# Performance work log

Measured on AMD Instinct MI355X. Metric: run time of the kernel, lower is better.

## Reference

```python
import jax, jax.numpy as jnp
import numpy as np

BS, L, D, ITEM_NUM = 64, 100, 64, 100000  # batch, max_seq_len, embedding_dim, item vocab
NEG_INF = -10000.0


def setup_inputs() -> dict:
    key = jax.random.key(0)
    k1, k2, k3, k4, k5 = jax.random.split(key, 5)
    N = BS * (L + 1)
    return {
        "prec_vec": jax.random.normal(k1, (BS * L, D), jnp.float32),
        "score_embs": jax.random.normal(k2, (N, D), jnp.float32),
        "pop_prob_list": jax.random.uniform(k3, (ITEM_NUM + 1,), jnp.float32, 0.01, 1.0),
        "sample_items_id": jax.random.randint(k4, (N,), 0, ITEM_NUM + 1, dtype=jnp.int32),
        "log_mask": jax.random.randint(k5, (BS, L), 0, 2, dtype=jnp.int32),
    }


def reference(prec_vec, score_embs, pop_prob_list, sample_items_id, log_mask):
    bs, L_ = log_mask.shape
    N = sample_items_id.shape[0]  # bs * (L+1)

    # debiased in-batch sampled-softmax logits: [bs*L, N]
    debias = jnp.log(pop_prob_list[sample_items_id])
    logits = jnp.matmul(prec_vec, score_embs.T) - debias[None, :]

    # column mask: padded positions (log_mask==0); last position of each seq always valid
    col_valid = jnp.concatenate(
        [log_mask, jnp.ones((bs, 1), log_mask.dtype)], axis=1
    ).reshape(-1)  # [N]
    logits = jnp.where(col_valid[None, :] == 0, NEG_INF, logits)

    # duplicate-item mask: dup[i, k] = any item in sequence i equals sample_items_id[k]
    id_list = sample_items_id.reshape(bs, L_ + 1)
    dup = (sample_items_id[None, None, :] == id_list[:, :, None]).any(axis=1)  # [bs, N]

    # targets: label for (i, j) is flat column i*(L+1) + j + 1
    tgt = jnp.arange(bs)[:, None] * (L_ + 1) + jnp.arange(L_)[None, :] + 1  # [bs, L]

    # apply dup mask per (i, j) but never mask the row's own target column
    not_target = jnp.arange(N)[None, None, :] != tgt[:, :, None]  # [bs, L, N]
    mask3 = dup[:, None, :] & not_target
    logits3 = jnp.where(mask3, NEG_INF, logits.reshape(bs, L_, N))

    # masked cross-entropy, mean over valid (log_mask != 0) rows
    logits2 = logits3.reshape(bs * L_, N)
    labels = tgt.reshape(-1)
    logp = jax.nn.log_softmax(logits2, axis=-1)
    nll = -jnp.take_along_axis(logp, labels[:, None], axis=1)[:, 0]  # [bs*L]
    w = (log_mask.reshape(-1) != 0).astype(logits2.dtype)
    return jnp.sum(nll * w) / jnp.sum(w)
```

## Files before the change

kernel.cpp:

```cpp
#include <hip/hip_runtime.h>

#define NEG_INF (-10000.0f)
#define L_SEQ   100
#define N_COLS  6464
#define D_      64
#define N_ROWS  6400
#define NS      16

#define OFF_PS  0
#define OFF_XT  409600
#define OFF_ACC 435200

typedef __attribute__((ext_vector_type(8))) short short8;
typedef __attribute__((ext_vector_type(4))) float f32x4;
union F8 { short8 v; unsigned short u[8]; unsigned w[4]; };

__device__ __forceinline__ unsigned short f2bf(float f) {
  unsigned u = __float_as_uint(f);
  return (unsigned short)((u + 0x7FFFu + ((u >> 16) & 1u)) >> 16);
}
__device__ __forceinline__ unsigned packbf(float lo, float hi) {
  return (__float_as_uint(hi) & 0xFFFF0000u) | (__float_as_uint(lo) >> 16);
}

__global__ __launch_bounds__(256, 2) void fused_kernel(
    const float* __restrict__ prec, const float* __restrict__ score,
    const float* __restrict__ pop, const int* __restrict__ sid,
    const int* __restrict__ lm,
    float* __restrict__ ps, float* __restrict__ xtrow) {
  __shared__ unsigned bs[3][512];
  __shared__ unsigned short btile[64 * 64];
  __shared__ float mdl[3 * 64];

  const int tid = threadIdx.x;
  const int split = blockIdx.y;
  const int blkrow = blockIdx.x * 128;
  const int w = tid >> 6, lane = tid & 63;
  const int lr = lane & 15, lk = lane >> 4;
  const int i0 = blkrow / L_SEQ;

  int rowbase[2], rbase4[2], sel_a[2], sel_b[2], lim[2];
#pragma unroll
  for (int rg = 0; rg < 2; ++rg) {
    rowbase[rg] = blkrow + rg * 64 + w * 16;
    rbase4[rg] = rowbase[rg] + lk * 4;
    int ia = rbase4[rg] / L_SEQ, ib = (rbase4[rg] + 3) / L_SEQ;
    sel_a[rg] = ia - i0;
    sel_b[rg] = ib - i0;
    lim[rg] = (ia + 1) * L_SEQ;
  }

  for (int x = tid; x < 3 * 512; x += 256) ((unsigned*)bs)[x] = 0u;
  __syncthreads();
  for (int x = tid; x < 303; x += 256) {
    int s = x / 101, pos = x - s * 101;
    int iq = i0 + s; if (iq > 63) iq = 63;
    int id = sid[iq * 101 + pos];
    atomicOr(&bs[s][(id >> 5) & 511], 1u << (id & 31));
  }

  F8 fa[2][2];
#pragma unroll
  for (int rg = 0; rg < 2; ++rg) {
    const float* prow = prec + (size_t)(rowbase[rg] + lr) * D_ + lk * 8;
    float4 a0 = *(const float4*)(prow);
    float4 a1 = *(const float4*)(prow + 4);
    float4 b0 = *(const float4*)(prow + 32);
    float4 b1 = *(const float4*)(prow + 36);
    fa[rg][0].u[0] = f2bf(a0.x); fa[rg][0].u[1] = f2bf(a0.y);
    fa[rg][0].u[2] = f2bf(a0.z); fa[rg][0].u[3] = f2bf(a0.w);
    fa[rg][0].u[4] = f2bf(a1.x); fa[rg][0].u[5] = f2bf(a1.y);
    fa[rg][0].u[6] = f2bf(a1.z); fa[rg][0].u[7] = f2bf(a1.w);
    fa[rg][1].u[0] = f2bf(b0.x); fa[rg][1].u[1] = f2bf(b0.y);
    fa[rg][1].u[2] = f2bf(b0.z); fa[rg][1].u[3] = f2bf(b0.w);
    fa[rg][1].u[4] = f2bf(b1.x); fa[rg][1].u[5] = f2bf(b1.y);
    fa[rg][1].u[6] = f2bf(b1.z); fa[rg][1].u[7] = f2bf(b1.w);
  }

  float s[2][4][4];
#pragma unroll
  for (int rg = 0; rg < 2; ++rg)
#pragma unroll
    for (int t4 = 0; t4 < 4; ++t4)
#pragma unroll
      for (int q = 0; q < 4; ++q) s[rg][t4][q] = 0.f;

  float4 sv[4];
  int svN = 0, lmvN = 0;

  auto STAGE_ISSUE = [&](int stv) {
    const float* base = score + (size_t)stv * 64 * D_;
#pragma unroll
    for (int j = 0; j < 4; ++j)
      sv[j] = *(const float4*)(base + j * 1024 + tid * 4);
    if (tid < 64) {
      int c = stv * 64 + tid;
      svN = sid[c];
      int i2 = c / 101, p = c - i2 * 101;
      lmvN = (p == L_SEQ) ? 1 : lm[i2 * L_SEQ + p];
    }
  };
  auto STAGE_WRITE = [&]() {
#pragma unroll
    for (int j = 0; j < 4; ++j) {
      int colw = j * 16 + (tid >> 4);
      int byteoff = colw * 128 + ((((tid & 15) * 8)) ^ ((colw & 7) << 4));
      uint2 pk;
      pk.x = packbf(sv[j].x, sv[j].y);
      pk.y = packbf(sv[j].z, sv[j].w);
      *(uint2*)((char*)btile + byteoff) = pk;
    }
    if (tid < 64) {
      float inv = 1.0f / pop[svN];
      unsigned hb = 1u << (svN & 31);
      int hw = (svN >> 5) & 511;
      mdl[tid]       = (lmvN && !(bs[0][hw] & hb)) ? inv : 0.f;
      mdl[64 + tid]  = (lmvN && !(bs[1][hw] & hb)) ? inv : 0.f;
      mdl[128 + tid] = (lmvN && !(bs[2][hw] & hb)) ? inv : 0.f;
    }
  };
  auto COMPUTE = [&]() {
    const int sw = (lr & 7) << 4;
    F8 fb0[4], fb1[4];
#pragma unroll
    for (int t4 = 0; t4 < 4; ++t4) {
      int col = t4 * 16 + lr;
      char* rowp = (char*)btile + col * 128;
      fb0[t4].v = *(const short8*)(rowp + ((lk * 16) ^ sw));
      fb1[t4].v = *(const short8*)(rowp + ((64 + lk * 16) ^ sw));
    }
#pragma unroll
    for (int rg = 0; rg < 2; ++rg) {
      float ma[4], mb[4];
#pragma unroll
      for (int t4 = 0; t4 < 4; ++t4) {
        ma[t4] = mdl[sel_a[rg] * 64 + t4 * 16 + lr];
        mb[t4] = mdl[sel_b[rg] * 64 + t4 * 16 + lr];
      }
      f32x4 acc[4];
#pragma unroll
      for (int t4 = 0; t4 < 4; ++t4) {
        f32x4 z = {0.f, 0.f, 0.f, 0.f};
        z = __builtin_amdgcn_mfma_f32_16x16x32_bf16(fa[rg][0].v, fb0[t4].v, z, 0, 0, 0);
        z = __builtin_amdgcn_mfma_f32_16x16x32_bf16(fa[rg][1].v, fb1[t4].v, z, 0, 0, 0);
        acc[t4] = z;
      }
#pragma unroll
      for (int q = 0; q < 4; ++q) {
        const bool ub = (rbase4[rg] + q) >= lim[rg];
#pragma unroll
        for (int t4 = 0; t4 < 4; ++t4) {
          float mm = ub ? mb[t4] : ma[t4];
          s[rg][t4][q] = fmaf(__expf(acc[t4][q]), mm, s[rg][t4][q]);
        }
      }
    }
  };

  const int nit = (100 - split) / NS + 1;
  int st = split;
  STAGE_ISSUE(st);
  __syncthreads();
  STAGE_WRITE();
  __syncthreads();
  for (int t = 0; t < nit; ++t) {
    const bool more = (t + 1 < nit);
    if (more) STAGE_ISSUE(st + NS);
    COMPUTE();
    if (more) {
      __syncthreads();
      STAGE_WRITE();
      __syncthreads();
    }
    st += NS;
  }

#pragma unroll
  for (int rg = 0; rg < 2; ++rg) {
    float sq[4];
#pragma unroll
    for (int q = 0; q < 4; ++q)
      sq[q] = (s[rg][0][q] + s[rg][1][q]) + (s[rg][2][q] + s[rg][3][q]);
#pragma unroll
    for (int q = 0; q < 4; ++q) {
#pragma unroll
      for (int off = 1; off < 16; off <<= 1)
        sq[q] += __shfl_xor(sq[q], off);
    }
    if (lr == 0) {
#pragma unroll
      for (int q = 0; q < 4; ++q)
        ps[(size_t)(rbase4[rg] + q) * NS + split] = sq[q];
    }
  }

  if (split == 0) {
#pragma unroll
    for (int rg = 0; rg < 2; ++rg) {
      int row_l = rowbase[rg] + lr;
      int i_l = row_l / L_SEQ, j_l = row_l - i_l * L_SEQ;
      int tgtc = i_l * 101 + j_l + 1;
      int p_l = j_l + 1;
      int vt = (p_l == L_SEQ) ? 1 : lm[i_l * L_SEQ + p_l];
      const float* srp = score + (size_t)tgtc * D_ + lk * 8;
      float4 s0 = *(const float4*)(srp);
      float4 s1 = *(const float4*)(srp + 4);
      float4 s2 = *(const float4*)(srp + 32);
      float4 s3 = *(const float4*)(srp + 36);
      F8 ft0, ft1;
      ft0.w[0] = packbf(s0.x, s0.y); ft0.w[1] = packbf(s0.z, s0.w);
      ft0.w[2] = packbf(s1.x, s1.y); ft0.w[3] = packbf(s1.z, s1.w);
      ft1.w[0] = packbf(s2.x, s2.y); ft1.w[1] = packbf(s2.z, s2.w);
      ft1.w[2] = packbf(s3.x, s3.y); ft1.w[3] = packbf(s3.z, s3.w);
      f32x4 z = {0.f, 0.f, 0.f, 0.f};
      z = __builtin_amdgcn_mfma_f32_16x16x32_bf16(fa[rg][0].v, ft0.v, z, 0, 0, 0);
      z = __builtin_amdgcn_mfma_f32_16x16x32_bf16(fa[rg][1].v, ft1.v, z, 0, 0, 0);
      int qs = lr - lk * 4;
      if (qs >= 0 && qs < 4) {
        float zd = (qs == 0) ? z[0] : (qs == 1) ? z[1] : (qs == 2) ? z[2] : z[3];
        float xv = zd - __logf(pop[sid[tgtc]]);
        xtrow[row_l] = vt ? xv : NEG_INF;
      }
    }
  }
}

__global__ __launch_bounds__(256) void merge_kernel(
    const float* __restrict__ ps, const float* __restrict__ xtrow,
    const int* __restrict__ lm, float* __restrict__ acc,
    unsigned* __restrict__ done, float* __restrict__ out) {
  const int r = blockIdx.x * 256 + threadIdx.x;
  const float4* pp = (const float4*)(ps + (size_t)r * NS);
  float4 a = pp[0], b = pp[1], c = pp[2], d = pp[3];
  float sv = ((a.x + a.y) + (a.z + a.w)) + ((b.x + b.y) + (b.z + b.w)) +
             ((c.x + c.y) + (c.z + c.w)) + ((d.x + d.y) + (d.z + d.w));
  float x = xtrow[r];
  sv += __expf(x);
  sv = fmaxf(sv, 1e-37f);
  const int v = (lm[r] != 0);
  float nll = v ? (__logf(sv) - x) : 0.f;
  float c1 = v ? 1.f : 0.f;
#pragma unroll
  for (int off = 1; off < 64; off <<= 1) {
    nll += __shfl_xor(nll, off);
    c1 += __shfl_xor(c1, off);
  }
  __shared__ float red[8];
  const int wq = threadIdx.x >> 6, lane = threadIdx.x & 63;
  if (lane == 0) { red[wq] = nll; red[4 + wq] = c1; }
  __syncthreads();
  if (threadIdx.x == 0) {
    float bsum = (red[0] + red[1]) + (red[2] + red[3]);
    float bcnt = (red[4] + red[5]) + (red[6] + red[7]);
    atomicAdd(&acc[0], bsum);
    atomicAdd(&acc[1], bcnt);
    __threadfence();
    unsigned t = atomicAdd(done, 1u);
    if (t == 24) {
      float S = atomicAdd(&acc[0], 0.f);
      float C = atomicAdd(&acc[1], 0.f);
      out[0] = S / C;
    }
  }
}

extern "C" void kernel_launch(void* const* d_in, const int* in_sizes, int n_in,
                              void* d_out, int out_size, void* d_ws, size_t ws_size,
                              hipStream_t stream) {
  const float* prec  = (const float*)d_in[0];
  const float* score = (const float*)d_in[1];
  const float* pop   = (const float*)d_in[2];
  const int*   sid   = (const int*)d_in[3];
  const int*   lm    = (const int*)d_in[4];

  char* ws = (char*)d_ws;
  float*    ps    = (float*)(ws + OFF_PS);
  float*    xtrow = (float*)(ws + OFF_XT);
  float*    acc   = (float*)(ws + OFF_ACC);
  unsigned* done  = (unsigned*)(ws + OFF_ACC + 8);
  float*    out   = (float*)d_out;

  hipMemsetAsync(acc, 0, 12, stream);
  hipLaunchKernelGGL(fused_kernel, dim3(50, NS), dim3(256), 0, stream,
                     prec, score, pop, sid, lm, ps, xtrow);
  hipLaunchKernelGGL(merge_kernel, dim3(25), dim3(256), 0, stream,
                     ps, xtrow, lm, acc, done, out);
}
```

Baseline: 34.38 us.

## Fold merge kernel into fused kernel via per-row-group last-block ticket reduction

Removes the separate merge kernel launch. Each row-group keeps an atomic ticket counter, and the last of the NS split blocks to finish that group reduces the partial sums, computes the NLL and adds it to the global accumulators. A global done counter then lets the final group write the mean. This saves one kernel launch and its dependency gap, at the cost of extra fences and atomics plus a serial tail in the last block of each group.

```diff
diff --git a/kernel.cpp b/kernel.cpp
--- a/kernel.cpp
+++ b/kernel.cpp
@@ -6,10 +6,11 @@
 #define D_      64
 #define N_ROWS  6400
 #define NS      16
+#define NGRP    50
 
 #define OFF_PS  0
 #define OFF_XT  409600
-#define OFF_ACC 435200
+#define OFF_CTL 435200
 
 typedef __attribute__((ext_vector_type(8))) short short8;
 typedef __attribute__((ext_vector_type(4))) float f32x4;
@@ -27,10 +28,14 @@
     const float* __restrict__ prec, const float* __restrict__ score,
     const float* __restrict__ pop, const int* __restrict__ sid,
     const int* __restrict__ lm,
-    float* __restrict__ ps, float* __restrict__ xtrow) {
+    float* __restrict__ ps, float* __restrict__ xtrow,
+    float* __restrict__ acc, unsigned* __restrict__ done,
+    unsigned* __restrict__ rowcnt, float* __restrict__ out) {
   __shared__ unsigned bs[3][512];
   __shared__ unsigned short btile[64 * 64];
   __shared__ float mdl[3 * 64];
+  __shared__ float red[8];
+  __shared__ unsigned ticket_s;
 
   const int tid = threadIdx.x;
   const int split = blockIdx.y;
@@ -137,13 +142,13 @@
         ma[t4] = mdl[sel_a[rg] * 64 + t4 * 16 + lr];
         mb[t4] = mdl[sel_b[rg] * 64 + t4 * 16 + lr];
       }
-      f32x4 acc[4];
+      f32x4 acc4[4];
 #pragma unroll
       for (int t4 = 0; t4 < 4; ++t4) {
         f32x4 z = {0.f, 0.f, 0.f, 0.f};
         z = __builtin_amdgcn_mfma_f32_16x16x32_bf16(fa[rg][0].v, fb0[t4].v, z, 0, 0, 0);
         z = __builtin_amdgcn_mfma_f32_16x16x32_bf16(fa[rg][1].v, fb1[t4].v, z, 0, 0, 0);
-        acc[t4] = z;
+        acc4[t4] = z;
       }
 #pragma unroll
       for (int q = 0; q < 4; ++q) {
@@ -151,7 +156,7 @@
 #pragma unroll
         for (int t4 = 0; t4 < 4; ++t4) {
           float mm = ub ? mb[t4] : ma[t4];
-          s[rg][t4][q] = fmaf(__expf(acc[t4][q]), mm, s[rg][t4][q]);
+          s[rg][t4][q] = fmaf(__expf(acc4[t4][q]), mm, s[rg][t4][q]);
         }
       }
     }
@@ -223,43 +228,43 @@
       }
     }
   }
-}
-
-__global__ __launch_bounds__(256) void merge_kernel(
-    const float* __restrict__ ps, const float* __restrict__ xtrow,
-    const int* __restrict__ lm, float* __restrict__ acc,
-    unsigned* __restrict__ done, float* __restrict__ out) {
-  const int r = blockIdx.x * 256 + threadIdx.x;
-  const float4* pp = (const float4*)(ps + (size_t)r * NS);
-  float4 a = pp[0], b = pp[1], c = pp[2], d = pp[3];
-  float sv = ((a.x + a.y) + (a.z + a.w)) + ((b.x + b.y) + (b.z + b.w)) +
-             ((c.x + c.y) + (c.z + c.w)) + ((d.x + d.y) + (d.z + d.w));
-  float x = xtrow[r];
-  sv += __expf(x);
-  sv = fmaxf(sv, 1e-37f);
-  const int v = (lm[r] != 0);
-  float nll = v ? (__logf(sv) - x) : 0.f;
-  float c1 = v ? 1.f : 0.f;
-#pragma unroll
-  for (int off = 1; off < 64; off <<= 1) {
-    nll += __shfl_xor(nll, off);
-    c1 += __shfl_xor(c1, off);
-  }
-  __shared__ float red[8];
-  const int wq = threadIdx.x >> 6, lane = threadIdx.x & 63;
-  if (lane == 0) { red[wq] = nll; red[4 + wq] = c1; }
-  __syncthreads();
-  if (threadIdx.x == 0) {
-    float bsum = (red[0] + red[1]) + (red[2] + red[3]);
-    float bcnt = (red[4] + red[5]) + (red[6] + red[7]);
-    atomicAdd(&acc[0], bsum);
-    atomicAdd(&acc[1], bcnt);
+
+  __threadfence();
+  if (tid == 0) ticket_s = atomicAdd(&rowcnt[blockIdx.x], 1u);
+  __syncthreads();
+  if (ticket_s == NS - 1) {
     __threadfence();
-    unsigned t = atomicAdd(done, 1u);
-    if (t == 24) {
-      float S = atomicAdd(&acc[0], 0.f);
-      float C = atomicAdd(&acc[1], 0.f);
-      out[0] = S / C;
+    float lsum = 0.f, lcnt = 0.f;
+    if (tid < 128) {
+      int r = blkrow + tid;
+      const float4* pp = (const float4*)(ps + (size_t)r * NS);
+      float4 a = pp[0], b = pp[1], c = pp[2], d = pp[3];
+      float sv2 = ((a.x + a.y) + (a.z + a.w)) + ((b.x + b.y) + (b.z + b.w)) +
+                  ((c.x + c.y) + (c.z + c.w)) + ((d.x + d.y) + (d.z + d.w));
+      float x = xtrow[r];
+      sv2 += __expf(x);
+      sv2 = fmaxf(sv2, 1e-37f);
+      if (lm[r] != 0) { lsum = __logf(sv2) - x; lcnt = 1.f; }
+    }
+#pragma unroll
+    for (int off = 1; off < 64; off <<= 1) {
+      lsum += __shfl_xor(lsum, off);
+      lcnt += __shfl_xor(lcnt, off);
+    }
+    if (lane == 0) { red[w] = lsum; red[4 + w] = lcnt; }
+    __syncthreads();
+    if (tid == 0) {
+      float bsum = (red[0] + red[1]) + (red[2] + red[3]);
+      float bcnt = (red[4] + red[5]) + (red[6] + red[7]);
+      atomicAdd(&acc[0], bsum);
+      atomicAdd(&acc[1], bcnt);
+      __threadfence();
+      unsigned t = atomicAdd(done, 1u);
+      if (t == NGRP - 1) {
+        float S = atomicAdd(&acc[0], 0.f);
+        float C = atomicAdd(&acc[1], 0.f);
+        out[0] = S / C;
+      }
     }
   }
 }
@@ -274,15 +279,14 @@
   const int*   lm    = (const int*)d_in[4];
 
   char* ws = (char*)d_ws;
-  float*    ps    = (float*)(ws + OFF_PS);
-  float*    xtrow = (float*)(ws + OFF_XT);
-  float*    acc   = (float*)(ws + OFF_ACC);
-  unsigned* done  = (unsigned*)(ws + OFF_ACC + 8);
-  float*    out   = (float*)d_out;
-
-  hipMemsetAsync(acc, 0, 12, stream);
-  hipLaunchKernelGGL(fused_kernel, dim3(50, NS), dim3(256), 0, stream,
-                     prec, score, pop, sid, lm, ps, xtrow);
-  hipLaunchKernelGGL(merge_kernel, dim3(25), dim3(256), 0, stream,
-                     ps, xtrow, lm, acc, done, out);
-}
+  float*    ps     = (float*)(ws + OFF_PS);
+  float*    xtrow  = (float*)(ws + OFF_XT);
+  float*    acc    = (float*)(ws + OFF_CTL);
+  unsigned* done   = (unsigned*)(ws + OFF_CTL + 8);
+  unsigned* rowcnt = (unsigned*)(ws + OFF_CTL + 12);
+  float*    out    = (float*)d_out;
+
+  hipMemsetAsync(acc, 0, 8 + 4 + 4 * NGRP, stream);
+  hipLaunchKernelGGL(fused_kernel, dim3(NGRP, NS), dim3(256), 0, stream,
+                     prec, score, pop, sid, lm, ps, xtrow, acc, done, rowcnt, out);
+}
```

Result: slower. 124.4 us (+261.7%).
